# Performance work log

Measured on AMD Instinct MI355X. Metric: run time of the kernel, lower is better.

The kernel has to match this reference:

```python
import jax, jax.numpy as jnp
import numpy as np

B, S, H, I, E = 1, 2048, 2048, 5632, 8
JITTER = 0.01
NEG = jnp.float32(-1e30)  # stands in for -inf; softmax prob underflows to 0


def setup_inputs() -> dict:
    key = jax.random.key(0)
    ks = jax.random.split(key, 5)
    return {
        "hidden_states": jax.random.normal(ks[0], (B, S, H), jnp.float32),
        "gate_w": jax.random.normal(ks[1], (E, H), jnp.float32) * 0.02,   # nn.Linear(H, E) weight
        "w1": jax.random.normal(ks[2], (E, I, H), jnp.float32) * 0.02,    # per-expert w1 weight [out=I, in=H]
        "w2": jax.random.normal(ks[3], (E, H, I), jnp.float32) * 0.02,    # per-expert w2 weight [out=H, in=I]
        "w3": jax.random.normal(ks[4], (E, I, H), jnp.float32) * 0.02,    # per-expert w3 weight [out=I, in=H]
    }


def _sparsemixer_top2(scores, jitter_eps):
    # masked_sampling_omp_inference: sparse-mixer top-2 routing
    top2, sel = jax.lax.top_k(scores, 2)                      # [T,2], [T,2]
    e = scores.shape[-1]
    # --- first expert multiplier ---
    m1 = top2[:, 0:1]                                         # [T,1]
    factor1 = jnp.maximum(jnp.abs(scores), m1)                # clamp(|s|, min=m1)
    mask1 = (m1 - scores) / factor1 > 2.0 * jitter_eps
    p1 = jax.nn.softmax(jnp.where(mask1, NEG, scores), axis=-1)
    mult1 = jnp.take_along_axis(p1, sel[:, 0:1], axis=-1)     # [T,1]
    # --- second expert multiplier (first expert knocked out) ---
    m2 = top2[:, 1:2]
    factor2 = jnp.maximum(jnp.abs(scores), m2)
    mask2 = (m2 - scores) / factor2 > 2.0 * jitter_eps
    onehot0 = sel[:, 0:1] == jnp.arange(e)[None, :]           # scatter(-inf) at top-1 index
    p2 = jax.nn.softmax(jnp.where(onehot0 | mask2, NEG, scores), axis=-1)
    mult2 = jnp.take_along_axis(p2, sel[:, 1:2], axis=-1)     # [T,1]
    return jnp.concatenate([mult1, mult2], axis=-1), sel       # [T,2], [T,2]


def reference(hidden_states, gate_w, w1, w2, w3):
    b, s, h = hidden_states.shape
    x = hidden_states.reshape(-1, h)                          # [T,H]
    logits = x @ gate_w.T                                     # [T,E] router logits
    mult, sel = _sparsemixer_top2(logits, JITTER)
    out = jnp.zeros_like(x)
    for e in range(w1.shape[0]):                              # fixed small expert count
        # combined routing weight for expert e (0 if not selected)
        we = jnp.sum(jnp.where(sel == e, mult, 0.0), axis=-1)  # [T]
        hid = jax.nn.silu(x @ w1[e].T) * (x @ w3[e].T)        # SwiGLU [T,I]
        out = out + we[:, None] * (hid @ w2[e].T)
    return out.reshape(b, s, h)
```

## Files before the change

kernel.cpp:

```cpp
#include <hip/hip_runtime.h>

#define TOKENS 2048
#define HDIM   2048
#define IDIM   5632
#define NEXP   8
#define NSLOT  (TOKENS * 2)
#define BM 128
#define BN 128
#define BK 32

typedef __attribute__((ext_vector_type(8))) short bf16x8;
typedef __attribute__((ext_vector_type(4))) float f32x4;

__device__ __forceinline__ unsigned short f2bf(float f) {
    union { float f; unsigned u; } v; v.f = f;
    unsigned r = v.u + 0x7FFFu + ((v.u >> 16) & 1u);
    return (unsigned short)(r >> 16);
}
__device__ __forceinline__ unsigned pack2(float lo, float hi) {
    return (unsigned)f2bf(lo) | ((unsigned)f2bf(hi) << 16);
}
__device__ __forceinline__ void stage_b_chunk(const float* __restrict__ p, unsigned short* dst) {
    float4 lo = *(const float4*)(p);
    float4 hi = *(const float4*)(p + 4);
    uint4 v;
    v.x = pack2(lo.x, lo.y);
    v.y = pack2(lo.z, lo.w);
    v.z = pack2(hi.x, hi.y);
    v.w = pack2(hi.z, hi.w);
    *(uint4*)dst = v;
}
__device__ __forceinline__ void gl2lds16(const void* g, void* l) {
    __builtin_amdgcn_global_load_lds(
        (const __attribute__((address_space(1))) unsigned int*)g,
        (__attribute__((address_space(3))) unsigned int*)l,
        16, 0, 0);
}

__global__ __launch_bounds__(256) void k_zero(float* __restrict__ out) {
    int i = blockIdx.x * 256 + threadIdx.x;
    float4 z = {0.f, 0.f, 0.f, 0.f};
    ((float4*)out)[i] = z;
}

__global__ __launch_bounds__(256) void k_cvt(const float* __restrict__ src,
                                             unsigned short* __restrict__ dst,
                                             int n8) {
    int stride = gridDim.x * 256;
    for (int i = blockIdx.x * 256 + threadIdx.x; i < n8; i += stride) {
        const float4* p = (const float4*)(src + (size_t)i * 8);
        float4 a = p[0], b = p[1];
        uint4 v;
        v.x = pack2(a.x, a.y); v.y = pack2(a.z, a.w);
        v.z = pack2(b.x, b.y); v.w = pack2(b.z, b.w);
        *(uint4*)(dst + (size_t)i * 8) = v;
    }
}

__global__ __launch_bounds__(256) void k_gate(const float* __restrict__ x,
                                              const float* __restrict__ gw,
                                              int* __restrict__ sel,
                                              float* __restrict__ wts) {
    int wave = threadIdx.x >> 6, lane = threadIdx.x & 63;
    int t = blockIdx.x * 4 + wave;
    const float4* xr = (const float4*)(x + (size_t)t * HDIM);
    const float4* g  = (const float4*)gw;
    float acc[NEXP];
#pragma unroll
    for (int e = 0; e < NEXP; e++) acc[e] = 0.f;
#pragma unroll
    for (int it = 0; it < HDIM / 4 / 64; ++it) {
        int idx = it * 64 + lane;
        float4 xv = xr[idx];
#pragma unroll
        for (int e = 0; e < NEXP; e++) {
            float4 gv = g[e * (HDIM / 4) + idx];
            acc[e] += xv.x * gv.x + xv.y * gv.y + xv.z * gv.z + xv.w * gv.w;
        }
    }
#pragma unroll
    for (int e = 0; e < NEXP; e++) {
        float v = acc[e];
#pragma unroll
        for (int off = 32; off > 0; off >>= 1) v += __shfl_xor(v, off, 64);
        acc[e] = v;
    }
    if (lane == 0) {
        float s[NEXP];
#pragma unroll
        for (int e = 0; e < NEXP; e++) s[e] = acc[e];
        float m1 = s[0]; int i1 = 0;
#pragma unroll
        for (int e = 1; e < NEXP; e++) if (s[e] > m1) { m1 = s[e]; i1 = e; }
        float m2 = -3.0e38f; int i2 = 0;
#pragma unroll
        for (int e = 0; e < NEXP; e++) if (e != i1 && s[e] > m2) { m2 = s[e]; i2 = e; }
        float sum1 = 0.f;
#pragma unroll
        for (int e = 0; e < NEXP; e++) {
            float f = fmaxf(fabsf(s[e]), m1);
            bool masked = ((m1 - s[e]) / f) > 0.02f;
            if (!masked) sum1 += expf(s[e] - m1);
        }
        float sum2 = 0.f;
#pragma unroll
        for (int e = 0; e < NEXP; e++) {
            if (e == i1) continue;
            float f = fmaxf(fabsf(s[e]), m2);
            bool masked = ((m2 - s[e]) / f) > 0.02f;
            if (!masked) sum2 += expf(s[e] - m2);
        }
        sel[2 * t]     = i1;
        sel[2 * t + 1] = i2;
        wts[2 * t]     = 1.f / sum1;
        wts[2 * t + 1] = 1.f / sum2;
    }
}

__global__ __launch_bounds__(256) void k_hist(const int* __restrict__ sel,
                                              int* __restrict__ cnt,
                                              int* __restrict__ offs,
                                              int* __restrict__ cursor) {
    __shared__ int c_s[NEXP];
    int tid = threadIdx.x;
    if (tid < NEXP) c_s[tid] = 0;
    __syncthreads();
    for (int i = tid; i < NSLOT; i += 256) atomicAdd(&c_s[sel[i]], 1);
    __syncthreads();
    if (tid == 0) {
        int o = 0;
        for (int e = 0; e < NEXP; e++) { cnt[e] = c_s[e]; offs[e] = o; o += c_s[e]; cursor[e] = 0; }
    }
}

__global__ __launch_bounds__(256) void k_gather(const float* __restrict__ x,
                                                const int* __restrict__ sel,
                                                const float* __restrict__ wts,
                                                const int* __restrict__ offs,
                                                int* __restrict__ cursor,
                                                int* __restrict__ rowtok,
                                                float* __restrict__ roww,
                                                int* __restrict__ tokslot,
                                                unsigned short* __restrict__ Xe) {
    int t = blockIdx.x;
    __shared__ int slot_s[2];
    if (threadIdx.x == 0) {
        int s0 = sel[2 * t], s1 = sel[2 * t + 1];
        int p0 = offs[s0] + atomicAdd(&cursor[s0], 1);
        int p1 = offs[s1] + atomicAdd(&cursor[s1], 1);
        rowtok[p0] = t; roww[p0] = wts[2 * t];
        rowtok[p1] = t; roww[p1] = wts[2 * t + 1];
        tokslot[2 * t] = p0; tokslot[2 * t + 1] = p1;
        slot_s[0] = p0; slot_s[1] = p1;
    }
    __syncthreads();
    int p0 = slot_s[0], p1 = slot_s[1];
    int base = threadIdx.x * 8;
    const float* xp = x + (size_t)t * HDIM + base;
    float4 a = *(const float4*)(xp);
    float4 b = *(const float4*)(xp + 4);
    uint4 v;
    v.x = pack2(a.x, a.y); v.y = pack2(a.z, a.w);
    v.z = pack2(b.x, b.y); v.w = pack2(b.z, b.w);
    *(uint4*)(Xe + (size_t)p0 * HDIM + base) = v;
    *(uint4*)(Xe + (size_t)p1 * HDIM + base) = v;
}


__global__ __launch_bounds__(256, 2) void k_ffn1_bf(const unsigned short* __restrict__ Xe,
                                                    const unsigned short* __restrict__ w1b,
                                                    const unsigned short* __restrict__ w3b,
                                                    const int* __restrict__ cnt,
                                                    const int* __restrict__ offs,
                                                    unsigned short* __restrict__ hid) {
    int e = blockIdx.z;
    int c = cnt[e];
    int bm = blockIdx.y;
    if (bm * BM >= c) return;
    int n0 = blockIdx.x * BN;
    int row0 = offs[e] + bm * BM;
    int rows_here = c - bm * BM;
    const unsigned short* W1 = w1b + (size_t)e * IDIM * HDIM;
    const unsigned short* W3 = w3b + (size_t)e * IDIM * HDIM;

    __shared__ __align__(16) unsigned short As[8 * 512];
    __shared__ __align__(16) unsigned short B1s[8 * 512];
    __shared__ __align__(16) unsigned short B3s[8 * 512];

    int tid = threadIdx.x, lane = tid & 63, wave = tid >> 6;
    int wm = wave >> 1, wn = wave & 1;
    int fr = lane & 15, kq = lane >> 4;

    f32x4 acc1[4][4], acc3[4][4];
    f32x4 z = {0.f, 0.f, 0.f, 0.f};
#pragma unroll
    for (int i = 0; i < 4; i++)
#pragma unroll
        for (int j = 0; j < 4; j++) { acc1[i][j] = z; acc3[i][j] = z; }

    int ar0 = min(row0 + wave * 16 + fr, NSLOT - 1);
    int ar1 = min(row0 + (wave + 4) * 16 + fr, NSLOT - 1);
    const unsigned short* aP0  = Xe + (size_t)ar0 * HDIM + kq * 8;
    const unsigned short* aP1  = Xe + (size_t)ar1 * HDIM + kq * 8;
    const unsigned short* b1P0 = W1 + (size_t)(n0 + wave * 16 + fr) * HDIM + kq * 8;
    const unsigned short* b1P1 = W1 + (size_t)(n0 + (wave + 4) * 16 + fr) * HDIM + kq * 8;
    const unsigned short* b3P0 = W3 + (size_t)(n0 + wave * 16 + fr) * HDIM + kq * 8;
    const unsigned short* b3P1 = W3 + (size_t)(n0 + (wave + 4) * 16 + fr) * HDIM + kq * 8;

    unsigned short* aL0  = As  + wave * 512;
    unsigned short* aL1  = As  + (wave + 4) * 512;
    unsigned short* b1L0 = B1s + wave * 512;
    unsigned short* b1L1 = B1s + (wave + 4) * 512;
    unsigned short* b3L0 = B3s + wave * 512;
    unsigned short* b3L1 = B3s + (wave + 4) * 512;

    for (int k0 = 0; k0 < HDIM; k0 += BK) {
        __syncthreads();
        gl2lds16(aP0 + k0, aL0);
        gl2lds16(aP1 + k0, aL1);
        gl2lds16(b1P0 + k0, b1L0);
        gl2lds16(b1P1 + k0, b1L1);
        gl2lds16(b3P0 + k0, b3L0);
        gl2lds16(b3P1 + k0, b3L1);
        __syncthreads();
        bf16x8 af[4];
#pragma unroll
        for (int i = 0; i < 4; i++)
            af[i] = *(const bf16x8*)&As[((wm * 4 + i) * 64 + lane) * 8];
#pragma unroll
        for (int j = 0; j < 4; j++) {
            bf16x8 b1f = *(const bf16x8*)&B1s[((wn * 4 + j) * 64 + lane) * 8];
            bf16x8 b3f = *(const bf16x8*)&B3s[((wn * 4 + j) * 64 + lane) * 8];
#pragma unroll
            for (int i = 0; i < 4; i++) {
                acc1[i][j] = __builtin_amdgcn_mfma_f32_16x16x32_bf16(af[i], b1f, acc1[i][j], 0, 0, 0);
                acc3[i][j] = __builtin_amdgcn_mfma_f32_16x16x32_bf16(af[i], b3f, acc3[i][j], 0, 0, 0);
            }
        }
    }
    int qr = (lane >> 4) * 4, cb = lane & 15;
#pragma unroll
    for (int i = 0; i < 4; i++) {
        int rl = wm * 64 + i * 16 + qr;
#pragma unroll
        for (int v = 0; v < 4; v++) {
            int r = rl + v;
            if (r < rows_here) {
                size_t rowoff = (size_t)(row0 + r) * IDIM;
#pragma unroll
                for (int j = 0; j < 4; j++) {
                    float u1 = acc1[i][j][v], u3 = acc3[i][j][v];
                    float h = u1 * u3 / (1.f + __expf(-u1));
                    hid[rowoff + n0 + wn * 64 + j * 16 + cb] = f2bf(h);
                }
            }
        }
    }
}

__global__ __launch_bounds__(256, 2) void k_ffn2_bf(const unsigned short* __restrict__ hid,
                                                    const unsigned short* __restrict__ w2b,
                                                    const int* __restrict__ cnt,
                                                    const int* __restrict__ offs,
                                                    const float* __restrict__ roww,
                                                    float* __restrict__ Oslot) {
    int e = blockIdx.z;
    int c = cnt[e];
    int bm = blockIdx.y;
    if (bm * BM >= c) return;
    int n0 = blockIdx.x * BN;
    int row0 = offs[e] + bm * BM;
    int rows_here = c - bm * BM;
    const unsigned short* W2 = w2b + (size_t)e * HDIM * IDIM;

    __shared__ __align__(16) unsigned short As[8 * 512];
    __shared__ __align__(16) unsigned short Bs[8 * 512];
    __shared__ float w_s[BM];

    int tid = threadIdx.x, lane = tid & 63, wave = tid >> 6;
    int wm = wave >> 1, wn = wave & 1;
    int fr = lane & 15, kq = lane >> 4;

    if (tid < BM) w_s[tid] = (tid < rows_here) ? roww[row0 + tid] : 0.f;

    f32x4 acc[4][4];
    f32x4 z = {0.f, 0.f, 0.f, 0.f};
#pragma unroll
    for (int i = 0; i < 4; i++)
#pragma unroll
        for (int j = 0; j < 4; j++) acc[i][j] = z;

    int ar0 = min(row0 + wave * 16 + fr, NSLOT - 1);
    int ar1 = min(row0 + (wave + 4) * 16 + fr, NSLOT - 1);
    const unsigned short* aP0 = hid + (size_t)ar0 * IDIM + kq * 8;
    const unsigned short* aP1 = hid + (size_t)ar1 * IDIM + kq * 8;
    const unsigned short* bP0 = W2 + (size_t)(n0 + wave * 16 + fr) * IDIM + kq * 8;
    const unsigned short* bP1 = W2 + (size_t)(n0 + (wave + 4) * 16 + fr) * IDIM + kq * 8;

    unsigned short* aL0 = As + wave * 512;
    unsigned short* aL1 = As + (wave + 4) * 512;
    unsigned short* bL0 = Bs + wave * 512;
    unsigned short* bL1 = Bs + (wave + 4) * 512;

    for (int k0 = 0; k0 < IDIM; k0 += BK) {
        __syncthreads();
        gl2lds16(aP0 + k0, aL0);
        gl2lds16(aP1 + k0, aL1);
        gl2lds16(bP0 + k0, bL0);
        gl2lds16(bP1 + k0, bL1);
        __syncthreads();
        bf16x8 af[4];
#pragma unroll
        for (int i = 0; i < 4; i++)
            af[i] = *(const bf16x8*)&As[((wm * 4 + i) * 64 + lane) * 8];
#pragma unroll
        for (int j = 0; j < 4; j++) {
            bf16x8 bf = *(const bf16x8*)&Bs[((wn * 4 + j) * 64 + lane) * 8];
#pragma unroll
            for (int i = 0; i < 4; i++)
                acc[i][j] = __builtin_amdgcn_mfma_f32_16x16x32_bf16(af[i], bf, acc[i][j], 0, 0, 0);
        }
    }
    int qr = (lane >> 4) * 4, cb = lane & 15;
#pragma unroll
    for (int i = 0; i < 4; i++) {
        int rl = wm * 64 + i * 16 + qr;
#pragma unroll
        for (int v = 0; v < 4; v++) {
            int r = rl + v;
            if (r < rows_here) {
                float wgt = w_s[r];
                float* orow = Oslot + (size_t)(row0 + r) * HDIM + n0 + wn * 64 + cb;
#pragma unroll
                for (int j = 0; j < 4; j++)
                    orow[j * 16] = acc[i][j][v] * wgt;
            }
        }
    }
}

__global__ __launch_bounds__(256) void k_combine(const float* __restrict__ Oslot,
                                                 const int* __restrict__ tokslot,
                                                 float* __restrict__ out) {
    int t = blockIdx.x;
    int p0 = tokslot[2 * t], p1 = tokslot[2 * t + 1];
    int i = threadIdx.x * 8;
    const float4* r0 = (const float4*)(Oslot + (size_t)p0 * HDIM + i);
    const float4* r1 = (const float4*)(Oslot + (size_t)p1 * HDIM + i);
    float4 a0 = r0[0], b0 = r0[1], a1 = r1[0], b1 = r1[1];
    float4 o0 = {a0.x + a1.x, a0.y + a1.y, a0.z + a1.z, a0.w + a1.w};
    float4 o1 = {b0.x + b1.x, b0.y + b1.y, b0.z + b1.z, b0.w + b1.w};
    float* op = out + (size_t)t * HDIM + i;
    *(float4*)op = o0;
    *(float4*)(op + 4) = o1;
}


__global__ __launch_bounds__(256, 2) void k_ffn1_cv(const unsigned short* __restrict__ Xe,
                                                    const float* __restrict__ w1,
                                                    const float* __restrict__ w3,
                                                    const int* __restrict__ cnt,
                                                    const int* __restrict__ offs,
                                                    unsigned short* __restrict__ hid) {
    int e = blockIdx.z;
    int c = cnt[e];
    int bm = blockIdx.y;
    if (bm * BM >= c) return;
    int n0 = blockIdx.x * BN;
    int row0 = offs[e] + bm * BM;
    int rows_here = c - bm * BM;
    const float* W1 = w1 + (size_t)e * IDIM * HDIM;
    const float* W3 = w3 + (size_t)e * IDIM * HDIM;

    __shared__ __align__(16) unsigned short As[8 * 512];
    __shared__ __align__(16) unsigned short B1s[8 * 512];
    __shared__ __align__(16) unsigned short B3s[8 * 512];

    int tid = threadIdx.x, lane = tid & 63, wave = tid >> 6;
    int wm = wave >> 1, wn = wave & 1;
    int fr = lane & 15, kq = lane >> 4;

    f32x4 acc1[4][4], acc3[4][4];
    f32x4 z = {0.f, 0.f, 0.f, 0.f};
#pragma unroll
    for (int i = 0; i < 4; i++)
#pragma unroll
        for (int j = 0; j < 4; j++) { acc1[i][j] = z; acc3[i][j] = z; }

    int ar0 = min(row0 + wave * 16 + fr, NSLOT - 1);
    int ar1 = min(row0 + (wave + 4) * 16 + fr, NSLOT - 1);
    const unsigned short* aP0 = Xe + (size_t)ar0 * HDIM + kq * 8;
    const unsigned short* aP1 = Xe + (size_t)ar1 * HDIM + kq * 8;
    const float* b1P0 = W1 + (size_t)(n0 + wave * 16 + fr) * HDIM + kq * 8;
    const float* b1P1 = W1 + (size_t)(n0 + (wave + 4) * 16 + fr) * HDIM + kq * 8;
    const float* b3P0 = W3 + (size_t)(n0 + wave * 16 + fr) * HDIM + kq * 8;
    const float* b3P1 = W3 + (size_t)(n0 + (wave + 4) * 16 + fr) * HDIM + kq * 8;

    for (int k0 = 0; k0 < HDIM; k0 += BK) {
        __syncthreads();
        *(uint4*)&As[(size_t)tid * 8]         = *(const uint4*)(aP0 + k0);
        *(uint4*)&As[(size_t)(tid + 256) * 8] = *(const uint4*)(aP1 + k0);
        stage_b_chunk(b1P0 + k0, &B1s[(size_t)tid * 8]);
        stage_b_chunk(b1P1 + k0, &B1s[(size_t)(tid + 256) * 8]);
        stage_b_chunk(b3P0 + k0, &B3s[(size_t)tid * 8]);
        stage_b_chunk(b3P1 + k0, &B3s[(size_t)(tid + 256) * 8]);
        __syncthreads();
        bf16x8 af[4];
#pragma unroll
        for (int i = 0; i < 4; i++)
            af[i] = *(const bf16x8*)&As[((wm * 4 + i) * 64 + lane) * 8];
#pragma unroll
        for (int j = 0; j < 4; j++) {
            bf16x8 b1f = *(const bf16x8*)&B1s[((wn * 4 + j) * 64 + lane) * 8];
            bf16x8 b3f = *(const bf16x8*)&B3s[((wn * 4 + j) * 64 + lane) * 8];
#pragma unroll
            for (int i = 0; i < 4; i++) {
                acc1[i][j] = __builtin_amdgcn_mfma_f32_16x16x32_bf16(af[i], b1f, acc1[i][j], 0, 0, 0);
                acc3[i][j] = __builtin_amdgcn_mfma_f32_16x16x32_bf16(af[i], b3f, acc3[i][j], 0, 0, 0);
            }
        }
    }
    int qr = (lane >> 4) * 4, cb = lane & 15;
#pragma unroll
    for (int i = 0; i < 4; i++) {
        int rl = wm * 64 + i * 16 + qr;
#pragma unroll
        for (int v = 0; v < 4; v++) {
            int r = rl + v;
            if (r < rows_here) {
                size_t rowoff = (size_t)(row0 + r) * IDIM;
#pragma unroll
                for (int j = 0; j < 4; j++) {
                    float u1 = acc1[i][j][v], u3 = acc3[i][j][v];
                    float h = u1 * u3 / (1.f + __expf(-u1));
                    hid[rowoff + n0 + wn * 64 + j * 16 + cb] = f2bf(h);
                }
            }
        }
    }
}

__global__ __launch_bounds__(256, 2) void k_ffn2_cv(const unsigned short* __restrict__ hid,
                                                    const float* __restrict__ w2,
                                                    const int* __restrict__ cnt,
                                                    const int* __restrict__ offs,
                                                    const int* __restrict__ rowtok,
                                                    const float* __restrict__ roww,
                                                    float* __restrict__ out) {
    int e = blockIdx.z;
    int c = cnt[e];
    int bm = blockIdx.y;
    if (bm * BM >= c) return;
    int n0 = blockIdx.x * BN;
    int row0 = offs[e] + bm * BM;
    int rows_here = c - bm * BM;
    const float* W2 = w2 + (size_t)e * HDIM * IDIM;

    __shared__ __align__(16) unsigned short As[8 * 512];
    __shared__ __align__(16) unsigned short Bs[8 * 512];
    __shared__ int   tok_s[BM];
    __shared__ float w_s[BM];

    int tid = threadIdx.x, lane = tid & 63, wave = tid >> 6;
    int wm = wave >> 1, wn = wave & 1;
    int fr = lane & 15, kq = lane >> 4;

    if (tid < BM) {
        bool valid = (tid < rows_here);
        tok_s[tid] = valid ? rowtok[row0 + tid] : 0;
        w_s[tid]   = valid ? roww[row0 + tid] : 0.f;
    }

    f32x4 acc[4][4];
    f32x4 z = {0.f, 0.f, 0.f, 0.f};
#pragma unroll
    for (int i = 0; i < 4; i++)
#pragma unroll
        for (int j = 0; j < 4; j++) acc[i][j] = z;

    int ar0 = min(row0 + wave * 16 + fr, NSLOT - 1);
    int ar1 = min(row0 + (wave + 4) * 16 + fr, NSLOT - 1);
    const unsigned short* aP0 = hid + (size_t)ar0 * IDIM + kq * 8;
    const unsigned short* aP1 = hid + (size_t)ar1 * IDIM + kq * 8;
    const float* bP0 = W2 + (size_t)(n0 + wave * 16 + fr) * IDIM + kq * 8;
    const float* bP1 = W2 + (size_t)(n0 + (wave + 4) * 16 + fr) * IDIM + kq * 8;

    for (int k0 = 0; k0 < IDIM; k0 += BK) {
        __syncthreads();
        *(uint4*)&As[(size_t)tid * 8]         = *(const uint4*)(aP0 + k0);
        *(uint4*)&As[(size_t)(tid + 256) * 8] = *(const uint4*)(aP1 + k0);
        stage_b_chunk(bP0 + k0, &Bs[(size_t)tid * 8]);
        stage_b_chunk(bP1 + k0, &Bs[(size_t)(tid + 256) * 8]);
        __syncthreads();
        bf16x8 af[4];
#pragma unroll
        for (int i = 0; i < 4; i++)
            af[i] = *(const bf16x8*)&As[((wm * 4 + i) * 64 + lane) * 8];
#pragma unroll
        for (int j = 0; j < 4; j++) {
            bf16x8 bf = *(const bf16x8*)&Bs[((wn * 4 + j) * 64 + lane) * 8];
#pragma unroll
            for (int i = 0; i < 4; i++)
                acc[i][j] = __builtin_amdgcn_mfma_f32_16x16x32_bf16(af[i], bf, acc[i][j], 0, 0, 0);
        }
    }
    int qr = (lane >> 4) * 4, cb = lane & 15;
#pragma unroll
    for (int i = 0; i < 4; i++) {
        int rl = wm * 64 + i * 16 + qr;
#pragma unroll
        for (int v = 0; v < 4; v++) {
            int r = rl + v;
            if (r < rows_here) {
                int tok = tok_s[r];
                float wgt = w_s[r];
                float* orow = out + (size_t)tok * HDIM + n0 + wn * 64 + cb;
#pragma unroll
                for (int j = 0; j < 4; j++)
                    atomicAdd(orow + j * 16, acc[i][j][v] * wgt);
            }
        }
    }
}

extern "C" void kernel_launch(void* const* d_in, const int* in_sizes, int n_in,
                              void* d_out, int out_size, void* d_ws, size_t ws_size,
                              hipStream_t stream) {
    const float* x  = (const float*)d_in[0];
    const float* gw = (const float*)d_in[1];
    const float* w1 = (const float*)d_in[2];
    const float* w2 = (const float*)d_in[3];
    const float* w3 = (const float*)d_in[4];
    float* out = (float*)d_out;

    char* ws = (char*)d_ws;
    int*   sel     = (int*)(ws);
    float* wts     = (float*)(ws + 16 * 1024);
    int*   cnt     = (int*)(ws + 32 * 1024);
    int*   offs    = (int*)(ws + 32 * 1024 + 256);
    int*   cursor  = (int*)(ws + 32 * 1024 + 512);
    int*   rowtok  = (int*)(ws + 48 * 1024);
    float* roww    = (float*)(ws + 64 * 1024);
    int*   tokslot = (int*)(ws + 80 * 1024);
    unsigned short* Xe  = (unsigned short*)(ws + (1ull << 20));
    unsigned short* hid = (unsigned short*)(ws + (18ull << 20));
    float*          Osl = (float*)(ws + (64ull << 20));
    unsigned short* w1b = (unsigned short*)(ws + (100ull << 20));
    unsigned short* w3b = (unsigned short*)(ws + (290ull << 20));
    unsigned short* w2b = w1b;

    const size_t EIH = (size_t)NEXP * IDIM * HDIM;
    const size_t REQ = (290ull << 20) + EIH * 2;

    k_gate<<<dim3(TOKENS / 4), dim3(256), 0, stream>>>(x, gw, sel, wts);
    k_hist<<<dim3(1), dim3(256), 0, stream>>>(sel, cnt, offs, cursor);
    k_gather<<<dim3(TOKENS), dim3(256), 0, stream>>>(x, sel, wts, offs, cursor, rowtok, roww, tokslot, Xe);

    if (ws_size >= REQ) {
        k_cvt<<<dim3(2048), dim3(256), 0, stream>>>(w1, w1b, (int)(EIH / 8));
        k_cvt<<<dim3(2048), dim3(256), 0, stream>>>(w3, w3b, (int)(EIH / 8));
        k_ffn1_bf<<<dim3(IDIM / BN, TOKENS / BM, NEXP), dim3(256), 0, stream>>>(Xe, w1b, w3b, cnt, offs, hid);
        k_cvt<<<dim3(2048), dim3(256), 0, stream>>>(w2, w2b, (int)(EIH / 8));
        k_ffn2_bf<<<dim3(HDIM / BN, TOKENS / BM, NEXP), dim3(256), 0, stream>>>(hid, w2b, cnt, offs, roww, Osl);
        k_combine<<<dim3(TOKENS), dim3(256), 0, stream>>>(Osl, tokslot, out);
    } else {
        k_zero<<<dim3((TOKENS * HDIM / 4) / 256), dim3(256), 0, stream>>>(out);
        k_ffn1_cv<<<dim3(IDIM / BN, TOKENS / BM, NEXP), dim3(256), 0, stream>>>(Xe, w1, w3, cnt, offs, hid);
        k_ffn2_cv<<<dim3(HDIM / BN, TOKENS / BM, NEXP), dim3(256), 0, stream>>>(hid, w2, cnt, offs, rowtok, roww, out);
    }
}
```

Before: 1.838 ms.

## Overlap w2 bf16 conversion with FFN1 and double K-step per barrier

Measured after the change: 1.797 ms. 1.02x faster.

```diff
diff --git a/kernel.cpp b/kernel.cpp
--- a/kernel.cpp
+++ b/kernel.cpp
@@ -172,7 +172,24 @@
                                                     const unsigned short* __restrict__ w3b,
                                                     const int* __restrict__ cnt,
                                                     const int* __restrict__ offs,
-                                                    unsigned short* __restrict__ hid) {
+                                                    unsigned short* __restrict__ hid,
+                                                    const float* __restrict__ w2src,
+                                                    unsigned short* __restrict__ w2dst) {
+    if (blockIdx.z == NEXP) {
+        int nblk = gridDim.x * gridDim.y;
+        int b = blockIdx.y * gridDim.x + blockIdx.x;
+        int n8 = (int)((size_t)NEXP * IDIM * HDIM / 8);
+        int stride = nblk * 256;
+        for (int i = b * 256 + threadIdx.x; i < n8; i += stride) {
+            const float4* p = (const float4*)(w2src + (size_t)i * 8);
+            float4 a = p[0], bb = p[1];
+            uint4 v;
+            v.x = pack2(a.x, a.y);  v.y = pack2(a.z, a.w);
+            v.z = pack2(bb.x, bb.y); v.w = pack2(bb.z, bb.w);
+            *(uint4*)(w2dst + (size_t)i * 8) = v;
+        }
+        return;
+    }
     int e = blockIdx.z;
     int c = cnt[e];
     int bm = blockIdx.y;
@@ -183,9 +200,9 @@
     const unsigned short* W1 = w1b + (size_t)e * IDIM * HDIM;
     const unsigned short* W3 = w3b + (size_t)e * IDIM * HDIM;
 
-    __shared__ __align__(16) unsigned short As[8 * 512];
-    __shared__ __align__(16) unsigned short B1s[8 * 512];
-    __shared__ __align__(16) unsigned short B3s[8 * 512];
+    __shared__ __align__(16) unsigned short As[16 * 512];
+    __shared__ __align__(16) unsigned short B1s[16 * 512];
+    __shared__ __align__(16) unsigned short B3s[16 * 512];
 
     int tid = threadIdx.x, lane = tid & 63, wave = tid >> 6;
     int wm = wave >> 1, wn = wave & 1;
@@ -214,7 +231,7 @@
     unsigned short* b3L0 = B3s + wave * 512;
     unsigned short* b3L1 = B3s + (wave + 4) * 512;
 
-    for (int k0 = 0; k0 < HDIM; k0 += BK) {
+    for (int k0 = 0; k0 < HDIM; k0 += 64) {
         __syncthreads();
         gl2lds16(aP0 + k0, aL0);
         gl2lds16(aP1 + k0, aL1);
@@ -222,19 +239,29 @@
         gl2lds16(b1P1 + k0, b1L1);
         gl2lds16(b3P0 + k0, b3L0);
         gl2lds16(b3P1 + k0, b3L1);
-        __syncthreads();
-        bf16x8 af[4];
-#pragma unroll
-        for (int i = 0; i < 4; i++)
-            af[i] = *(const bf16x8*)&As[((wm * 4 + i) * 64 + lane) * 8];
-#pragma unroll
-        for (int j = 0; j < 4; j++) {
-            bf16x8 b1f = *(const bf16x8*)&B1s[((wn * 4 + j) * 64 + lane) * 8];
-            bf16x8 b3f = *(const bf16x8*)&B3s[((wn * 4 + j) * 64 + lane) * 8];
-#pragma unroll
-            for (int i = 0; i < 4; i++) {
-                acc1[i][j] = __builtin_amdgcn_mfma_f32_16x16x32_bf16(af[i], b1f, acc1[i][j], 0, 0, 0);
-                acc3[i][j] = __builtin_amdgcn_mfma_f32_16x16x32_bf16(af[i], b3f, acc3[i][j], 0, 0, 0);
+        gl2lds16(aP0 + k0 + 32, aL0 + 4096);
+        gl2lds16(aP1 + k0 + 32, aL1 + 4096);
+        gl2lds16(b1P0 + k0 + 32, b1L0 + 4096);
+        gl2lds16(b1P1 + k0 + 32, b1L1 + 4096);
+        gl2lds16(b3P0 + k0 + 32, b3L0 + 4096);
+        gl2lds16(b3P1 + k0 + 32, b3L1 + 4096);
+        __syncthreads();
+#pragma unroll
+        for (int h = 0; h < 2; h++) {
+            int hb = h * 4096;
+            bf16x8 af[4];
+#pragma unroll
+            for (int i = 0; i < 4; i++)
+                af[i] = *(const bf16x8*)&As[hb + ((wm * 4 + i) * 64 + lane) * 8];
+#pragma unroll
+            for (int j = 0; j < 4; j++) {
+                bf16x8 b1f = *(const bf16x8*)&B1s[hb + ((wn * 4 + j) * 64 + lane) * 8];
+                bf16x8 b3f = *(const bf16x8*)&B3s[hb + ((wn * 4 + j) * 64 + lane) * 8];
+#pragma unroll
+                for (int i = 0; i < 4; i++) {
+                    acc1[i][j] = __builtin_amdgcn_mfma_f32_16x16x32_bf16(af[i], b1f, acc1[i][j], 0, 0, 0);
+                    acc3[i][j] = __builtin_amdgcn_mfma_f32_16x16x32_bf16(af[i], b3f, acc3[i][j], 0, 0, 0);
+                }
             }
         }
     }
@@ -273,8 +300,8 @@
     int rows_here = c - bm * BM;
     const unsigned short* W2 = w2b + (size_t)e * HDIM * IDIM;
 
-    __shared__ __align__(16) unsigned short As[8 * 512];
-    __shared__ __align__(16) unsigned short Bs[8 * 512];
+    __shared__ __align__(16) unsigned short As[16 * 512];
+    __shared__ __align__(16) unsigned short Bs[16 * 512];
     __shared__ float w_s[BM];
 
     int tid = threadIdx.x, lane = tid & 63, wave = tid >> 6;
@@ -302,23 +329,31 @@
     unsigned short* bL0 = Bs + wave * 512;
     unsigned short* bL1 = Bs + (wave + 4) * 512;
 
-    for (int k0 = 0; k0 < IDIM; k0 += BK) {
+    for (int k0 = 0; k0 < IDIM; k0 += 64) {
         __syncthreads();
         gl2lds16(aP0 + k0, aL0);
         gl2lds16(aP1 + k0, aL1);
         gl2lds16(bP0 + k0, bL0);
         gl2lds16(bP1 + k0, bL1);
-        __syncthreads();
-        bf16x8 af[4];
-#pragma unroll
-        for (int i = 0; i < 4; i++)
-            af[i] = *(const bf16x8*)&As[((wm * 4 + i) * 64 + lane) * 8];
-#pragma unroll
-        for (int j = 0; j < 4; j++) {
-            bf16x8 bf = *(const bf16x8*)&Bs[((wn * 4 + j) * 64 + lane) * 8];
+        gl2lds16(aP0 + k0 + 32, aL0 + 4096);
+        gl2lds16(aP1 + k0 + 32, aL1 + 4096);
+        gl2lds16(bP0 + k0 + 32, bL0 + 4096);
+        gl2lds16(bP1 + k0 + 32, bL1 + 4096);
+        __syncthreads();
+#pragma unroll
+        for (int h = 0; h < 2; h++) {
+            int hb = h * 4096;
+            bf16x8 af[4];
 #pragma unroll
             for (int i = 0; i < 4; i++)
-                acc[i][j] = __builtin_amdgcn_mfma_f32_16x16x32_bf16(af[i], bf, acc[i][j], 0, 0, 0);
+                af[i] = *(const bf16x8*)&As[hb + ((wm * 4 + i) * 64 + lane) * 8];
+#pragma unroll
+            for (int j = 0; j < 4; j++) {
+                bf16x8 bf = *(const bf16x8*)&Bs[hb + ((wn * 4 + j) * 64 + lane) * 8];
+#pragma unroll
+                for (int i = 0; i < 4; i++)
+                    acc[i][j] = __builtin_amdgcn_mfma_f32_16x16x32_bf16(af[i], bf, acc[i][j], 0, 0, 0);
+            }
         }
     }
     int qr = (lane >> 4) * 4, cb = lane & 15;
@@ -547,20 +582,30 @@
     float*          Osl = (float*)(ws + (64ull << 20));
     unsigned short* w1b = (unsigned short*)(ws + (100ull << 20));
     unsigned short* w3b = (unsigned short*)(ws + (290ull << 20));
-    unsigned short* w2b = w1b;
-
-    const size_t EIH = (size_t)NEXP * IDIM * HDIM;
-    const size_t REQ = (290ull << 20) + EIH * 2;
+    unsigned short* w2sep = (unsigned short*)(ws + (480ull << 20));
+
+    const size_t EIH  = (size_t)NEXP * IDIM * HDIM;
+    const size_t REQ1 = (290ull << 20) + EIH * 2;
+    const size_t REQ2 = (480ull << 20) + EIH * 2;
 
     k_gate<<<dim3(TOKENS / 4), dim3(256), 0, stream>>>(x, gw, sel, wts);
     k_hist<<<dim3(1), dim3(256), 0, stream>>>(sel, cnt, offs, cursor);
     k_gather<<<dim3(TOKENS), dim3(256), 0, stream>>>(x, sel, wts, offs, cursor, rowtok, roww, tokslot, Xe);
 
-    if (ws_size >= REQ) {
+    if (ws_size >= REQ1) {
+        bool sep = (ws_size >= REQ2);
+        unsigned short* w2b = sep ? w2sep : w1b;
+
         k_cvt<<<dim3(2048), dim3(256), 0, stream>>>(w1, w1b, (int)(EIH / 8));
         k_cvt<<<dim3(2048), dim3(256), 0, stream>>>(w3, w3b, (int)(EIH / 8));
-        k_ffn1_bf<<<dim3(IDIM / BN, TOKENS / BM, NEXP), dim3(256), 0, stream>>>(Xe, w1b, w3b, cnt, offs, hid);
-        k_cvt<<<dim3(2048), dim3(256), 0, stream>>>(w2, w2b, (int)(EIH / 8));
+        if (sep) {
+            k_ffn1_bf<<<dim3(IDIM / BN, TOKENS / BM, NEXP + 1), dim3(256), 0, stream>>>(
+                Xe, w1b, w3b, cnt, offs, hid, w2, w2b);
+        } else {
+            k_ffn1_bf<<<dim3(IDIM / BN, TOKENS / BM, NEXP), dim3(256), 0, stream>>>(
+                Xe, w1b, w3b, cnt, offs, hid, nullptr, nullptr);
+            k_cvt<<<dim3(2048), dim3(256), 0, stream>>>(w2, w2b, (int)(EIH / 8));
+        }
         k_ffn2_bf<<<dim3(HDIM / BN, TOKENS / BM, NEXP), dim3(256), 0, stream>>>(hid, w2b, cnt, offs, roww, Osl);
         k_combine<<<dim3(TOKENS), dim3(256), 0, stream>>>(Osl, tokslot, out);
     } else {
```

## Fuse fp32-to-bf16 weight conversion into FFN GEMM tile loading

Applied to the files above, without the earlier changes.

Measured after the change: 1.866 ms. About the same (+1.5%).

```diff
diff --git a/kernel.cpp b/kernel.cpp
--- a/kernel.cpp
+++ b/kernel.cpp
@@ -1,4 +1,5 @@
 #include <hip/hip_runtime.h>
+#include <hip/hip_bf16.h>
 
 #define TOKENS 2048
 #define HDIM   2048
@@ -18,7 +19,10 @@
     return (unsigned short)(r >> 16);
 }
 __device__ __forceinline__ unsigned pack2(float lo, float hi) {
-    return (unsigned)f2bf(lo) | ((unsigned)f2bf(hi) << 16);
+    float2 f; f.x = lo; f.y = hi;
+    __hip_bfloat162 h = __float22bfloat162_rn(f);
+    union { __hip_bfloat162 h; unsigned u; } c; c.h = h;
+    return c.u;
 }
 __device__ __forceinline__ void stage_b_chunk(const float* __restrict__ p, unsigned short* dst) {
     float4 lo = *(const float4*)(p);
@@ -41,20 +45,6 @@
     int i = blockIdx.x * 256 + threadIdx.x;
     float4 z = {0.f, 0.f, 0.f, 0.f};
     ((float4*)out)[i] = z;
-}
-
-__global__ __launch_bounds__(256) void k_cvt(const float* __restrict__ src,
-                                             unsigned short* __restrict__ dst,
-                                             int n8) {
-    int stride = gridDim.x * 256;
-    for (int i = blockIdx.x * 256 + threadIdx.x; i < n8; i += stride) {
-        const float4* p = (const float4*)(src + (size_t)i * 8);
-        float4 a = p[0], b = p[1];
-        uint4 v;
-        v.x = pack2(a.x, a.y); v.y = pack2(a.z, a.w);
-        v.z = pack2(b.x, b.y); v.w = pack2(b.z, b.w);
-        *(uint4*)(dst + (size_t)i * 8) = v;
-    }
 }
 
 __global__ __launch_bounds__(256) void k_gate(const float* __restrict__ x,
@@ -168,8 +158,8 @@
 
 
 __global__ __launch_bounds__(256, 2) void k_ffn1_bf(const unsigned short* __restrict__ Xe,
-                                                    const unsigned short* __restrict__ w1b,
-                                                    const unsigned short* __restrict__ w3b,
+                                                    const float* __restrict__ w1,
+                                                    const float* __restrict__ w3,
                                                     const int* __restrict__ cnt,
                                                     const int* __restrict__ offs,
                                                     unsigned short* __restrict__ hid) {
@@ -180,16 +170,17 @@
     int n0 = blockIdx.x * BN;
     int row0 = offs[e] + bm * BM;
     int rows_here = c - bm * BM;
-    const unsigned short* W1 = w1b + (size_t)e * IDIM * HDIM;
-    const unsigned short* W3 = w3b + (size_t)e * IDIM * HDIM;
-
-    __shared__ __align__(16) unsigned short As[8 * 512];
-    __shared__ __align__(16) unsigned short B1s[8 * 512];
-    __shared__ __align__(16) unsigned short B3s[8 * 512];
+    const float* W1 = w1 + (size_t)e * IDIM * HDIM;
+    const float* W3 = w3 + (size_t)e * IDIM * HDIM;
+
+    __shared__ __align__(16) unsigned short As[16 * 512];
+    __shared__ __align__(16) unsigned short B1s[16 * 512];
+    __shared__ __align__(16) unsigned short B3s[16 * 512];
 
     int tid = threadIdx.x, lane = tid & 63, wave = tid >> 6;
     int wm = wave >> 1, wn = wave & 1;
     int fr = lane & 15, kq = lane >> 4;
+    int lo8 = lane * 8;
 
     f32x4 acc1[4][4], acc3[4][4];
     f32x4 z = {0.f, 0.f, 0.f, 0.f};
@@ -200,41 +191,51 @@
 
     int ar0 = min(row0 + wave * 16 + fr, NSLOT - 1);
     int ar1 = min(row0 + (wave + 4) * 16 + fr, NSLOT - 1);
-    const unsigned short* aP0  = Xe + (size_t)ar0 * HDIM + kq * 8;
-    const unsigned short* aP1  = Xe + (size_t)ar1 * HDIM + kq * 8;
-    const unsigned short* b1P0 = W1 + (size_t)(n0 + wave * 16 + fr) * HDIM + kq * 8;
-    const unsigned short* b1P1 = W1 + (size_t)(n0 + (wave + 4) * 16 + fr) * HDIM + kq * 8;
-    const unsigned short* b3P0 = W3 + (size_t)(n0 + wave * 16 + fr) * HDIM + kq * 8;
-    const unsigned short* b3P1 = W3 + (size_t)(n0 + (wave + 4) * 16 + fr) * HDIM + kq * 8;
+    const unsigned short* aP0 = Xe + (size_t)ar0 * HDIM + kq * 8;
+    const unsigned short* aP1 = Xe + (size_t)ar1 * HDIM + kq * 8;
+    const float* b1P0 = W1 + (size_t)(n0 + wave * 16 + fr) * HDIM + kq * 8;
+    const float* b1P1 = W1 + (size_t)(n0 + (wave + 4) * 16 + fr) * HDIM + kq * 8;
+    const float* b3P0 = W3 + (size_t)(n0 + wave * 16 + fr) * HDIM + kq * 8;
+    const float* b3P1 = W3 + (size_t)(n0 + (wave + 4) * 16 + fr) * HDIM + kq * 8;
 
     unsigned short* aL0  = As  + wave * 512;
     unsigned short* aL1  = As  + (wave + 4) * 512;
-    unsigned short* b1L0 = B1s + wave * 512;
-    unsigned short* b1L1 = B1s + (wave + 4) * 512;
-    unsigned short* b3L0 = B3s + wave * 512;
-    unsigned short* b3L1 = B3s + (wave + 4) * 512;
-
-    for (int k0 = 0; k0 < HDIM; k0 += BK) {
+    unsigned short* b1D0 = B1s + wave * 512 + lo8;
+    unsigned short* b1D1 = B1s + (wave + 4) * 512 + lo8;
+    unsigned short* b3D0 = B3s + wave * 512 + lo8;
+    unsigned short* b3D1 = B3s + (wave + 4) * 512 + lo8;
+
+    for (int k0 = 0; k0 < HDIM; k0 += 64) {
         __syncthreads();
         gl2lds16(aP0 + k0, aL0);
         gl2lds16(aP1 + k0, aL1);
-        gl2lds16(b1P0 + k0, b1L0);
-        gl2lds16(b1P1 + k0, b1L1);
-        gl2lds16(b3P0 + k0, b3L0);
-        gl2lds16(b3P1 + k0, b3L1);
-        __syncthreads();
-        bf16x8 af[4];
-#pragma unroll
-        for (int i = 0; i < 4; i++)
-            af[i] = *(const bf16x8*)&As[((wm * 4 + i) * 64 + lane) * 8];
-#pragma unroll
-        for (int j = 0; j < 4; j++) {
-            bf16x8 b1f = *(const bf16x8*)&B1s[((wn * 4 + j) * 64 + lane) * 8];
-            bf16x8 b3f = *(const bf16x8*)&B3s[((wn * 4 + j) * 64 + lane) * 8];
-#pragma unroll
-            for (int i = 0; i < 4; i++) {
-                acc1[i][j] = __builtin_amdgcn_mfma_f32_16x16x32_bf16(af[i], b1f, acc1[i][j], 0, 0, 0);
-                acc3[i][j] = __builtin_amdgcn_mfma_f32_16x16x32_bf16(af[i], b3f, acc3[i][j], 0, 0, 0);
+        gl2lds16(aP0 + k0 + 32, aL0 + 4096);
+        gl2lds16(aP1 + k0 + 32, aL1 + 4096);
+        stage_b_chunk(b1P0 + k0,      b1D0);
+        stage_b_chunk(b1P1 + k0,      b1D1);
+        stage_b_chunk(b1P0 + k0 + 32, b1D0 + 4096);
+        stage_b_chunk(b1P1 + k0 + 32, b1D1 + 4096);
+        stage_b_chunk(b3P0 + k0,      b3D0);
+        stage_b_chunk(b3P1 + k0,      b3D1);
+        stage_b_chunk(b3P0 + k0 + 32, b3D0 + 4096);
+        stage_b_chunk(b3P1 + k0 + 32, b3D1 + 4096);
+        __syncthreads();
+#pragma unroll
+        for (int h = 0; h < 2; h++) {
+            int hb = h * 4096;
+            bf16x8 af[4];
+#pragma unroll
+            for (int i = 0; i < 4; i++)
+                af[i] = *(const bf16x8*)&As[hb + ((wm * 4 + i) * 64 + lane) * 8];
+#pragma unroll
+            for (int j = 0; j < 4; j++) {
+                bf16x8 b1f = *(const bf16x8*)&B1s[hb + ((wn * 4 + j) * 64 + lane) * 8];
+                bf16x8 b3f = *(const bf16x8*)&B3s[hb + ((wn * 4 + j) * 64 + lane) * 8];
+#pragma unroll
+                for (int i = 0; i < 4; i++) {
+                    acc1[i][j] = __builtin_amdgcn_mfma_f32_16x16x32_bf16(af[i], b1f, acc1[i][j], 0, 0, 0);
+                    acc3[i][j] = __builtin_amdgcn_mfma_f32_16x16x32_bf16(af[i], b3f, acc3[i][j], 0, 0, 0);
+                }
             }
         }
     }
@@ -259,7 +260,7 @@
 }
 
 __global__ __launch_bounds__(256, 2) void k_ffn2_bf(const unsigned short* __restrict__ hid,
-                                                    const unsigned short* __restrict__ w2b,
+                                                    const float* __restrict__ w2,
                                                     const int* __restrict__ cnt,
                                                     const int* __restrict__ offs,
                                                     const float* __restrict__ roww,
@@ -271,15 +272,16 @@
     int n0 = blockIdx.x * BN;
     int row0 = offs[e] + bm * BM;
     int rows_here = c - bm * BM;
-    const unsigned short* W2 = w2b + (size_t)e * HDIM * IDIM;
-
-    __shared__ __align__(16) unsigned short As[8 * 512];
-    __shared__ __align__(16) unsigned short Bs[8 * 512];
+    const float* W2 = w2 + (size_t)e * HDIM * IDIM;
+
+    __shared__ __align__(16) unsigned short As[16 * 512];
+    __shared__ __align__(16) unsigned short Bs[16 * 512];
     __shared__ float w_s[BM];
 
     int tid = threadIdx.x, lane = tid & 63, wave = tid >> 6;
     int wm = wave >> 1, wn = wave & 1;
     int fr = lane & 15, kq = lane >> 4;
+    int lo8 = lane * 8;
 
     if (tid < BM) w_s[tid] = (tid < rows_here) ? roww[row0 + tid] : 0.f;
 
@@ -294,31 +296,39 @@
     int ar1 = min(row0 + (wave + 4) * 16 + fr, NSLOT - 1);
     const unsigned short* aP0 = hid + (size_t)ar0 * IDIM + kq * 8;
     const unsigned short* aP1 = hid + (size_t)ar1 * IDIM + kq * 8;
-    const unsigned short* bP0 = W2 + (size_t)(n0 + wave * 16 + fr) * IDIM + kq * 8;
-    const unsigned short* bP1 = W2 + (size_t)(n0 + (wave + 4) * 16 + fr) * IDIM + kq * 8;
+    const float* bP0 = W2 + (size_t)(n0 + wave * 16 + fr) * IDIM + kq * 8;
+    const float* bP1 = W2 + (size_t)(n0 + (wave + 4) * 16 + fr) * IDIM + kq * 8;
 
     unsigned short* aL0 = As + wave * 512;
     unsigned short* aL1 = As + (wave + 4) * 512;
-    unsigned short* bL0 = Bs + wave * 512;
-    unsigned short* bL1 = Bs + (wave + 4) * 512;
-
-    for (int k0 = 0; k0 < IDIM; k0 += BK) {
+    unsigned short* bD0 = Bs + wave * 512 + lo8;
+    unsigned short* bD1 = Bs + (wave + 4) * 512 + lo8;
+
+    for (int k0 = 0; k0 < IDIM; k0 += 64) {
         __syncthreads();
         gl2lds16(aP0 + k0, aL0);
         gl2lds16(aP1 + k0, aL1);
-        gl2lds16(bP0 + k0, bL0);
-        gl2lds16(bP1 + k0, bL1);
-        __syncthreads();
-        bf16x8 af[4];
-#pragma unroll
-        for (int i = 0; i < 4; i++)
-            af[i] = *(const bf16x8*)&As[((wm * 4 + i) * 64 + lane) * 8];
-#pragma unroll
-        for (int j = 0; j < 4; j++) {
-            bf16x8 bf = *(const bf16x8*)&Bs[((wn * 4 + j) * 64 + lane) * 8];
+        gl2lds16(aP0 + k0 + 32, aL0 + 4096);
+        gl2lds16(aP1 + k0 + 32, aL1 + 4096);
+        stage_b_chunk(bP0 + k0,      bD0);
+        stage_b_chunk(bP1 + k0,      bD1);
+        stage_b_chunk(bP0 + k0 + 32, bD0 + 4096);
+        stage_b_chunk(bP1 + k0 + 32, bD1 + 4096);
+        __syncthreads();
+#pragma unroll
+        for (int h = 0; h < 2; h++) {
+            int hb = h * 4096;
+            bf16x8 af[4];
 #pragma unroll
             for (int i = 0; i < 4; i++)
-                acc[i][j] = __builtin_amdgcn_mfma_f32_16x16x32_bf16(af[i], bf, acc[i][j], 0, 0, 0);
+                af[i] = *(const bf16x8*)&As[hb + ((wm * 4 + i) * 64 + lane) * 8];
+#pragma unroll
+            for (int j = 0; j < 4; j++) {
+                bf16x8 bf = *(const bf16x8*)&Bs[hb + ((wn * 4 + j) * 64 + lane) * 8];
+#pragma unroll
+                for (int i = 0; i < 4; i++)
+                    acc[i][j] = __builtin_amdgcn_mfma_f32_16x16x32_bf16(af[i], bf, acc[i][j], 0, 0, 0);
+            }
         }
     }
     int qr = (lane >> 4) * 4, cb = lane & 15;
@@ -545,23 +555,16 @@
     unsigned short* Xe  = (unsigned short*)(ws + (1ull << 20));
     unsigned short* hid = (unsigned short*)(ws + (18ull << 20));
     float*          Osl = (float*)(ws + (64ull << 20));
-    unsigned short* w1b = (unsigned short*)(ws + (100ull << 20));
-    unsigned short* w3b = (unsigned short*)(ws + (290ull << 20));
-    unsigned short* w2b = w1b;
-
-    const size_t EIH = (size_t)NEXP * IDIM * HDIM;
-    const size_t REQ = (290ull << 20) + EIH * 2;
+
+    const size_t REQ_FAST = (64ull << 20) + (size_t)NSLOT * HDIM * sizeof(float);
 
     k_gate<<<dim3(TOKENS / 4), dim3(256), 0, stream>>>(x, gw, sel, wts);
     k_hist<<<dim3(1), dim3(256), 0, stream>>>(sel, cnt, offs, cursor);
     k_gather<<<dim3(TOKENS), dim3(256), 0, stream>>>(x, sel, wts, offs, cursor, rowtok, roww, tokslot, Xe);
 
-    if (ws_size >= REQ) {
-        k_cvt<<<dim3(2048), dim3(256), 0, stream>>>(w1, w1b, (int)(EIH / 8));
-        k_cvt<<<dim3(2048), dim3(256), 0, stream>>>(w3, w3b, (int)(EIH / 8));
-        k_ffn1_bf<<<dim3(IDIM / BN, TOKENS / BM, NEXP), dim3(256), 0, stream>>>(Xe, w1b, w3b, cnt, offs, hid);
-        k_cvt<<<dim3(2048), dim3(256), 0, stream>>>(w2, w2b, (int)(EIH / 8));
-        k_ffn2_bf<<<dim3(HDIM / BN, TOKENS / BM, NEXP), dim3(256), 0, stream>>>(hid, w2b, cnt, offs, roww, Osl);
+    if (ws_size >= REQ_FAST) {
+        k_ffn1_bf<<<dim3(IDIM / BN, TOKENS / BM, NEXP), dim3(256), 0, stream>>>(Xe, w1, w3, cnt, offs, hid);
+        k_ffn2_bf<<<dim3(HDIM / BN, TOKENS / BM, NEXP), dim3(256), 0, stream>>>(hid, w2, cnt, offs, roww, Osl);
         k_combine<<<dim3(TOKENS), dim3(256), 0, stream>>>(Osl, tokslot, out);
     } else {
         k_zero<<<dim3((TOKENS * HDIM / 4) / 256), dim3(256), 0, stream>>>(out);
```
